# Kernel tuning notes

Measured on AMD Instinct MI355X. Metric: run time of the kernel, lower is better.

Reference implementation:

```python
import jax, jax.numpy as jnp
import numpy as np
import math

B, S, E, H = 2, 2048, 1024, 16
HD = E // H          # head_dim = 64
HX = 64              # helix_dim
P = HX // 2          # helix pairs = 32

def setup_inputs() -> dict:
    key = jax.random.key(0)
    ks = jax.random.split(key, 12)
    sc = 0.02
    return {
        "x":    jax.random.normal(ks[0], (B, S, E), dtype=jnp.float32),
        "Wq":   jax.random.normal(ks[1], (E, E), dtype=jnp.float32) * sc,
        "bq":   jnp.zeros((E,), dtype=jnp.float32),
        "Wk":   jax.random.normal(ks[2], (E, E), dtype=jnp.float32) * sc,
        "bk":   jnp.zeros((E,), dtype=jnp.float32),
        "Wv":   jax.random.normal(ks[3], (E, E), dtype=jnp.float32) * sc,
        "bv":   jnp.zeros((E,), dtype=jnp.float32),
        "Wo":   jax.random.normal(ks[4], (E, E), dtype=jnp.float32) * sc,
        "bo":   jnp.zeros((E,), dtype=jnp.float32),
        "Whel": jax.random.normal(ks[5], (H, HX, HD), dtype=jnp.float32) * sc,
        "bhel": jnp.zeros((H, HX), dtype=jnp.float32),
    }

def _l2norm(x, eps=1e-12):
    # torch F.normalize(p=2, dim=-1): x / max(||x||, eps)
    n = jnp.sqrt(jnp.sum(x * x, axis=-1, keepdims=True))
    return x / jnp.maximum(n, eps)

def _scramble(t):
    # faithful to torch: (B,S,2) -> transpose(1,2) -> reshape(B,S,2),
    # vectorized over (H,P): t is (B,H,P,S,2)
    b, h, p, s, _ = t.shape
    return jnp.swapaxes(t, -1, -2).reshape(b, h, p, s, 2)

def reference(x, Wq, bq, Wk, bk, Wv, bv, Wo, bo, Whel, bhel):
    b, s, e = x.shape
    h, hx, hd = Whel.shape
    p = hx // 2
    q = x @ Wq.T + bq
    k = x @ Wk.T + bk
    v = x @ Wv.T + bv
    qh = q.reshape(b, s, h, hd)
    kh = k.reshape(b, s, h, hd)
    # per-head helical projections: (B,S,H,HX)
    q_hel = jnp.einsum('bshd,hed->bshe', qh, Whel) + bhel
    k_hel = jnp.einsum('bshd,hed->bshe', kh, Whel) + bhel
    # split into 2D coords, normalize each pair: (B,H,P,S,2)
    qn = _l2norm(q_hel.reshape(b, s, h, p, 2)).transpose(0, 2, 3, 1, 4)
    kn = _l2norm(k_hel.reshape(b, s, h, p, 2)).transpose(0, 2, 3, 1, 4)
    qn = _scramble(qn)
    kn = _scramble(kn)
    # helical similarity averaged over pairs: (B,H,S,S)
    helical = jnp.einsum('bhpsc,bhptc->bhst', qn, kn) / p
    # standard scaled dot-product scores
    dot = jnp.einsum('bshd,bthd->bhst', qh, kh) / math.sqrt(hd)
    alpha = 0.5
    attn = jax.nn.softmax(alpha * dot + (1.0 - alpha) * helical, axis=-1)
    vh = v.reshape(b, s, h, hd)
    out = jnp.einsum('bhst,bthd->bshd', attn, vh).reshape(b, s, e)
    return out @ Wo.T + bo
```

## Files before the change

### kernel.cpp

```cpp
#include <hip/hip_runtime.h>
#include <hip/hip_bf16.h>


typedef unsigned short u16;
typedef unsigned int u32;
typedef __attribute__((ext_vector_type(8))) __bf16 bf16x8;
typedef __attribute__((ext_vector_type(4))) float f32x4;
typedef __attribute__((ext_vector_type(16))) float f32x16;

union BFrag { u32 u[4]; bf16x8 b; };

__device__ __forceinline__ u16 f2b(float f) {
  u32 u = __float_as_uint(f);
  u32 r = (u + 0x7fffu + ((u >> 16) & 1u)) >> 16;
  return (u16)r;
}
__device__ __forceinline__ float b2f(u16 h) {
  return __uint_as_float(((u32)h) << 16);
}

__device__ __forceinline__ f32x4 mfma16(bf16x8 a, bf16x8 b, f32x4 c) {
  return __builtin_amdgcn_mfma_f32_16x16x32_bf16(a, b, c, 0, 0, 0);
}
__device__ __forceinline__ f32x16 mfma32(bf16x8 a, bf16x8 b, f32x16 c) {
  return __builtin_amdgcn_mfma_f32_32x32x16_bf16(a, b, c, 0, 0, 0);
}

__device__ __forceinline__ void gld16(void* lds, const void* g) {
  __builtin_amdgcn_global_load_lds(
      (const __attribute__((address_space(1))) unsigned int*)g,
      (__attribute__((address_space(3))) unsigned int*)lds, 16, 0, 0);
}

__device__ __forceinline__ void pl32swap(u32& a, u32& b, int l5) {
#if __has_builtin(__builtin_amdgcn_permlane32_swap)
  typedef unsigned int u32x2v __attribute__((ext_vector_type(2)));
  u32x2v r = __builtin_amdgcn_permlane32_swap(a, b, false, false);
  a = r[0];
  b = r[1];
#else
  u32 ea = __shfl_xor((int)a, 32);
  u32 eb = __shfl_xor((int)b, 32);
  u32 na = l5 ? eb : a;
  u32 nb = l5 ? b : ea;
  a = na;
  b = nb;
#endif
}

#define LOG2E 1.4426950408889634f

#define PIPE_BARRIER(N)                                         \
  do {                                                          \
    __builtin_amdgcn_sched_barrier(0);                          \
    asm volatile("s_waitcnt vmcnt(" #N ")" ::: "memory");       \
    __builtin_amdgcn_s_barrier();                               \
    __builtin_amdgcn_sched_barrier(0);                          \
  } while (0)

__global__ __launch_bounds__(256) void cast_kernel(
    const float* __restrict__ x,  const float* __restrict__ wq,
    const float* __restrict__ wk, const float* __restrict__ wv,
    const float* __restrict__ wo, const float* __restrict__ whel,
    u16* __restrict__ xb, u16* __restrict__ wb, u16* __restrict__ wob,
    u16* __restrict__ whb) {
  long long q = (long long)blockIdx.x * 256 + threadIdx.x;
  const float* s; u16* d; long long base;
  if (q < 1048576)      { s = x;    d = xb;            base = 0; }
  else if (q < 1310720) { s = wq;   d = wb;            base = 1048576; }
  else if (q < 1572864) { s = wk;   d = wb + 1048576;  base = 1310720; }
  else if (q < 1835008) { s = wv;   d = wb + 2097152;  base = 1572864; }
  else if (q < 2097152) { s = wo;   d = wob;           base = 1835008; }
  else                  { s = whel; d = whb;           base = 2097152; }
  long long e = (q - base) * 4;
  float4 v = *(const float4*)(s + e);
  ushort4 o;
  o.x = f2b(v.x); o.y = f2b(v.y); o.z = f2b(v.z); o.w = f2b(v.w);
  *(ushort4*)(d + e) = o;
}

__global__ __launch_bounds__(512, 6) void qkv_gemm(
    const u16* __restrict__ xb, const u16* __restrict__ wb,
    const float* __restrict__ bq, const float* __restrict__ bk,
    const float* __restrict__ bv, const u16* __restrict__ whb,
    const float* __restrict__ bhel,
    u16* __restrict__ Qcat, u16* __restrict__ Kcat, u16* __restrict__ vt) {
  union SM {
    struct { u16 Al[3][128][32]; u16 Bl[3][128][32]; } m;
    struct { u16 T[64][136]; } t;
    struct { u16 Th[4][32][72]; u16 Hs[2][128][64]; } e;
  };
  __shared__ SM sm;
  const int nt = blockIdx.x, mt = blockIdx.y;
  const int which = nt >> 3;
  const int n0 = (nt & 7) << 7;
  const int m0 = mt << 7;
  const int tid = threadIdx.x;
  const int w = tid >> 6, lane = tid & 63;
  const int g = lane >> 4, c15 = lane & 15;
  const int wm = w & 1, hl = (w >> 1) & 1, ch = w >> 2;
  const int nbase = hl * 64 + ch * 32;
  const u16* Wp = wb + (long long)which * (1024 * 1024) + n0 * 1024;
  const u16* Ap = xb + m0 * 1024;
  const int srow = tid >> 2;
  const int scol = (tid & 3) << 3;

  f32x4 acc[4][2];
#pragma unroll
  for (int i = 0; i < 4; i++)
#pragma unroll
    for (int j = 0; j < 2; j++) acc[i][j] = f32x4{0.f, 0.f, 0.f, 0.f};

  gld16(&sm.m.Al[0][srow][scol], Ap + srow * 1024 + scol);
  gld16(&sm.m.Bl[0][srow][scol], Wp + srow * 1024 + scol);
  gld16(&sm.m.Al[1][srow][scol], Ap + srow * 1024 + 32 + scol);
  gld16(&sm.m.Bl[1][srow][scol], Wp + srow * 1024 + 32 + scol);

  int cur = 0;
  for (int it = 0; it < 32; ++it) {
    if (it < 31) { PIPE_BARRIER(2); } else { PIPE_BARRIER(0); }
    if (it + 2 < 32) {
      const int pf = (cur >= 1) ? cur - 1 : 2;
      const int kn = (it + 2) << 5;
      gld16(&sm.m.Al[pf][srow][scol], Ap + srow * 1024 + kn + scol);
      gld16(&sm.m.Bl[pf][srow][scol], Wp + srow * 1024 + kn + scol);
    }
    bf16x8 a[4], b[2];
#pragma unroll
    for (int i = 0; i < 4; i++)
      a[i] = *(const bf16x8*)&sm.m.Al[cur][wm * 64 + i * 16 + c15][g * 8];
#pragma unroll
    for (int j = 0; j < 2; j++)
      b[j] = *(const bf16x8*)&sm.m.Bl[cur][nbase + j * 16 + c15][g * 8];
#pragma unroll
    for (int i = 0; i < 4; i++)
#pragma unroll
      for (int j = 0; j < 2; j++) acc[i][j] = mfma16(a[i], b[j], acc[i][j]);
    cur = (cur == 2) ? 0 : cur + 1;
  }

  if (which == 2) {
#pragma unroll
    for (int half = 0; half < 2; ++half) {
      __syncthreads();
      if (hl == half) {
#pragma unroll
        for (int i = 0; i < 4; i++)
#pragma unroll
          for (int j = 0; j < 2; j++)
#pragma unroll
            for (int r = 0; r < 4; r++) {
              int nloc = ch * 32 + j * 16 + c15;
              int mloc = wm * 64 + i * 16 + g * 4 + r;
              float v = acc[i][j][r] + bv[n0 + half * 64 + nloc];
              sm.t.T[nloc][mloc] = f2b(v);
            }
      }
      __syncthreads();
#pragma unroll
      for (int it = 0; it < 2; ++it) {
        int idx = it * 512 + tid;
        int row = idx >> 4;
        int cm = (idx & 15) * 8;
        int col = n0 + half * 64 + row;
        int hh = col >> 6, dd = col & 63;
        int m = m0 + cm;
        int bb2 = m >> 11, s = m & 2047;
        *(uint4*)&vt[(((bb2 * 16 + hh) * 64) + dd) * 2048 + s] =
            *(const uint4*)&sm.t.T[row][cm];
      }
    }
    return;
  }

  const float* bias = (which == 0) ? bq : bk;
  const float fold = (which == 0) ? (0.0625f * LOG2E) : 1.0f;
  const float osc  = (which == 0) ? (0.125f * LOG2E) : 0.125f;
  const int h0 = n0 >> 6;
  const int hsel = h0 + hl;
  const int pid = hl * 2 + wm;
  u16* Dst = ((which == 0) ? Qcat : Kcat);

  __syncthreads();
  const int bb2 = m0 >> 11;
  const int ubase = (m0 & 2047) >> 1;

#pragma unroll
  for (int half = 0; half < 2; ++half) {
#pragma unroll
    for (int i2 = 0; i2 < 2; ++i2) {
      int i = half * 2 + i2;
#pragma unroll
      for (int j = 0; j < 2; ++j)
#pragma unroll
        for (int r = 0; r < 4; ++r) {
          int row = m0 + wm * 64 + i * 16 + g * 4 + r;
          int d = ch * 32 + j * 16 + c15;
          int col = n0 + hl * 64 + d;
          float vraw = acc[i][j][r] + bias[col];
          int bb = row >> 11, s = row & 2047;
          Dst[(((long long)(bb * 16 + hsel) * 2048) + s) * 128 + d] =
              f2b(vraw * fold);
          sm.e.Th[pid][i2 * 16 + g * 4 + r][d] = f2b(vraw);
        }
    }
    __syncthreads();

    bf16x8 wf[2][4];
#pragma unroll
    for (int kh = 0; kh < 2; ++kh)
#pragma unroll
      for (int nf = 0; nf < 4; ++nf)
        wf[kh][nf] = *(const bf16x8*)(whb + hsel * 4096 +
                                      (nf * 16 + c15) * 64 + kh * 32 + g * 8);

    f32x4 hacc[4];
#pragma unroll
    for (int nf = 0; nf < 4; ++nf) hacc[nf] = f32x4{0.f, 0.f, 0.f, 0.f};
#pragma unroll
    for (int kh = 0; kh < 2; ++kh) {
      bf16x8 a0 = *(const bf16x8*)&sm.e.Th[pid][ch * 16 + c15][kh * 32 + g * 8];
#pragma unroll
      for (int nf = 0; nf < 4; ++nf)
        hacc[nf] = mfma16(a0, wf[kh][nf], hacc[nf]);
    }
#pragma unroll
    for (int nf = 0; nf < 4; ++nf)
#pragma unroll
      for (int r = 0; r < 4; ++r) {
        int e = nf * 16 + c15;
        float v = hacc[nf][r] + bhel[hsel * 64 + e];
        float pp = __shfl_xor(v, 1);
        float nn = sqrtf(v * v + pp * pp);
        float o = v / fmaxf(nn, 1e-12f) * osc;
        int tl = wm * 64 + half * 32 + ch * 16 + g * 4 + r;
        sm.e.Hs[hl][(e & 1) * 64 + (tl >> 1)][(e & ~1) | (tl & 1)] = f2b(o);
      }
    __syncthreads();
  }
#pragma unroll
  for (int it = 0; it < 4; ++it) {
    int idx = it * 512 + tid;
    int hh = idx >> 10;
    int hr = (idx >> 3) & 127;
    int ck = idx & 7;
    int coord = hr >> 6, ul = hr & 63;
    int row_out = coord * 1024 + ubase + ul;
    *(uint4*)&Dst[(((long long)(bb2 * 16 + h0 + hh) * 2048) + row_out) * 128 +
                  64 + ck * 8] = *(const uint4*)&sm.e.Hs[hh][hr][ck * 8];
  }
}

__global__ __launch_bounds__(512, 4) void attn_kernel(
    const u16* __restrict__ Qcat, const u16* __restrict__ Kcat,
    const u16* __restrict__ vt, u16* __restrict__ AO) {
  __shared__ u16 Kl[3][64][128];
  __shared__ u16 Vl[3][64][64];
  __shared__ float denl[2][128];
  const int bh = blockIdx.x, qt = blockIdx.y;
  const int bb = bh >> 4, h = bh & 15;
  const int q0 = qt << 7;
  const int tid = threadIdx.x;
  const int w = tid >> 6, lane = tid & 63;
  const int wq = w & 3, wt = w >> 2;
  const int l31 = lane & 31, l5 = lane >> 5;
  const u16* Qb = Qcat + (long long)bh * (2048 * 128);
  const u16* Kb = Kcat + (long long)bh * (2048 * 128);
  const u16* Vb = vt + (long long)bh * (64 * 2048);

  bf16x8 qf[8];
  {
    const u16* qrow = Qb + (q0 + 32 * wq + l31) * 128 + l5 * 8;
#pragma unroll
    for (int ks = 0; ks < 8; ++ks) qf[ks] = *(const bf16x8*)(qrow + ks * 16);
  }

  const int ll = tid;
  const int krow0 = ll >> 4;
  const int kp = ll & 15;
  const int ksrc0 = (kp & 8) | ((kp & 7) ^ (krow0 & 7));
  const int krow1 = 32 + krow0;
  const int ksrc1 = (kp & 8) | ((kp & 7) ^ (krow1 & 7));
  const int vd = ll >> 3;
  const int vsrc = (ll & 7) ^ (vd & 7);

  gld16(((u16*)Kl[0]) + ll * 8,        Kb + krow0 * 128 + ksrc0 * 8);
  gld16(((u16*)Kl[0]) + 4096 + ll * 8, Kb + krow1 * 128 + ksrc1 * 8);
  gld16(((u16*)Vl[0]) + ll * 8,        Vb + vd * 2048 + vsrc * 8);
  gld16(((u16*)Kl[1]) + ll * 8,        Kb + (64 + krow0) * 128 + ksrc0 * 8);
  gld16(((u16*)Kl[1]) + 4096 + ll * 8, Kb + (64 + krow1) * 128 + ksrc1 * 8);
  gld16(((u16*)Vl[1]) + ll * 8,        Vb + vd * 2048 + 64 + vsrc * 8);

  f32x16 accO0, accO1;
#pragma unroll
  for (int i = 0; i < 16; ++i) { accO0[i] = 0.f; accO1[i] = 0.f; }
  float den = 0.f;

  const int krow = 32 * wt + l31;
  const int kr7 = krow & 7;

  int cur = 0;
  for (int t = 0; t < 32; ++t) {
    if (t < 31) { PIPE_BARRIER(3); } else { PIPE_BARRIER(0); }
    if (t + 2 < 32) {
      const int pf = (cur >= 1) ? cur - 1 : 2;
      const int t2 = (t + 2) << 6;
      u16* Kd = (u16*)Kl[pf];
      gld16(Kd + ll * 8,        Kb + (t2 + krow0) * 128 + ksrc0 * 8);
      gld16(Kd + 4096 + ll * 8, Kb + (t2 + krow1) * 128 + ksrc1 * 8);
      gld16(((u16*)Vl[pf]) + ll * 8, Vb + vd * 2048 + t2 + vsrc * 8);
    }

    f32x16 accS;
#pragma unroll
    for (int i = 0; i < 16; ++i) accS[i] = 0.f;
#pragma unroll
    for (int ks = 0; ks < 8; ++ks) {
      int lc = 2 * ks + l5;
      int p = (lc & 8) | ((lc & 7) ^ kr7);
      bf16x8 ak = *(const bf16x8*)&Kl[cur][krow][p * 8];
      accS = mfma32(ak, qf[ks], accS);
    }

    u32 D0[2], D1[2], D2[2], D3[2];
#pragma unroll
    for (int rr = 0; rr < 4; ++rr) {
      float p0 = __builtin_amdgcn_exp2f(accS[4 * rr + 0]);
      float p1 = __builtin_amdgcn_exp2f(accS[4 * rr + 1]);
      float p2 = __builtin_amdgcn_exp2f(accS[4 * rr + 2]);
      float p3 = __builtin_amdgcn_exp2f(accS[4 * rr + 3]);
      den += (p0 + p1) + (p2 + p3);
      u32 lo = __builtin_amdgcn_perm(__float_as_uint(p1), __float_as_uint(p0),
                                     0x07060302u);
      u32 hi = __builtin_amdgcn_perm(__float_as_uint(p3), __float_as_uint(p2),
                                     0x07060302u);
      if (rr == 0) { D0[0] = lo; D0[1] = hi; }
      else if (rr == 1) { D1[0] = lo; D1[1] = hi; }
      else if (rr == 2) { D2[0] = lo; D2[1] = hi; }
      else { D3[0] = lo; D3[1] = hi; }
    }
    BFrag A0, A1;
    A0.u[0] = D0[0]; A0.u[2] = D1[0]; pl32swap(A0.u[0], A0.u[2], l5);
    A0.u[1] = D0[1]; A0.u[3] = D1[1]; pl32swap(A0.u[1], A0.u[3], l5);
    A1.u[0] = D2[0]; A1.u[2] = D3[0]; pl32swap(A1.u[0], A1.u[2], l5);
    A1.u[1] = D2[1]; A1.u[3] = D3[1]; pl32swap(A1.u[1], A1.u[3], l5);

#pragma unroll
    for (int dq = 0; dq < 2; ++dq) {
      int d = 32 * dq + l31;
      int d7 = d & 7;
#pragma unroll
      for (int ks = 0; ks < 2; ++ks) {
        int lc = 4 * wt + 2 * ks + l5;
        bf16x8 bvf = *(const bf16x8*)&Vl[cur][d][((lc ^ d7) & 7) * 8];
        if (dq == 0) accO0 = mfma32(ks ? A1.b : A0.b, bvf, accO0);
        else         accO1 = mfma32(ks ? A1.b : A0.b, bvf, accO1);
      }
    }
    cur = (cur == 2) ? 0 : cur + 1;
  }

  den += __shfl_xor(den, 32);
  if (lane < 32) denl[wt][32 * wq + lane] = den;
  __syncthreads();

  float* S = (float*)Kl;
  if (wt == 1) {
#pragma unroll
    for (int r = 0; r < 16; ++r) {
      int qr = (r & 3) + 8 * (r >> 2) + 4 * l5;
      S[(wq * 32 + qr) * 64 + l31] = accO0[r];
      S[(wq * 32 + qr) * 64 + 32 + l31] = accO1[r];
    }
  }
  __syncthreads();
  if (wt == 0) {
#pragma unroll
    for (int r = 0; r < 16; ++r) {
      int qr = (r & 3) + 8 * (r >> 2) + 4 * l5;
      int ql = 32 * wq + qr;
      float inv = 1.0f / (denl[0][ql] + denl[1][ql]);
      float o0 = (accO0[r] + S[(wq * 32 + qr) * 64 + l31]) * inv;
      float o1 = (accO1[r] + S[(wq * 32 + qr) * 64 + 32 + l31]) * inv;
      long long base = ((long long)(bb * 2048 + q0 + ql) * 1024) + h * 64;
      AO[base + l31] = f2b(o0);
      AO[base + 32 + l31] = f2b(o1);
    }
  }
}

__global__ __launch_bounds__(256, 4) void out_gemm(
    const u16* __restrict__ AO, const u16* __restrict__ wob,
    const float* __restrict__ bo, float* __restrict__ out) {
  __shared__ u16 Al[3][64][32];
  __shared__ u16 Bl[3][64][32];
  const int n0 = blockIdx.x << 6;
  const int m0 = blockIdx.y << 6;
  const int tid = threadIdx.x;
  const int wave = tid >> 6, lane = tid & 63;
  const int g = lane >> 4, c15 = lane & 15;
  const int wm = wave & 1, wn = wave >> 1;
  const u16* Wp = wob + n0 * 1024;
  const u16* Ap = AO + m0 * 1024;
  const int srow = tid >> 2;
  const int scol = (tid & 3) << 3;

  f32x4 acc[2][2];
#pragma unroll
  for (int i = 0; i < 2; i++)
#pragma unroll
    for (int j = 0; j < 2; j++) acc[i][j] = f32x4{0.f, 0.f, 0.f, 0.f};

  gld16(&Al[0][srow][scol], Ap + srow * 1024 + scol);
  gld16(&Bl[0][srow][scol], Wp + srow * 1024 + scol);
  gld16(&Al[1][srow][scol], Ap + srow * 1024 + 32 + scol);
  gld16(&Bl[1][srow][scol], Wp + srow * 1024 + 32 + scol);

  int cur = 0;
  for (int it = 0; it < 32; ++it) {
    if (it < 31) { PIPE_BARRIER(2); } else { PIPE_BARRIER(0); }
    if (it + 2 < 32) {
      const int pf = (cur >= 1) ? cur - 1 : 2;
      const int kn = (it + 2) << 5;
      gld16(&Al[pf][srow][scol], Ap + srow * 1024 + kn + scol);
      gld16(&Bl[pf][srow][scol], Wp + srow * 1024 + kn + scol);
    }
    bf16x8 a[2], b[2];
#pragma unroll
    for (int i = 0; i < 2; i++)
      a[i] = *(const bf16x8*)&Al[cur][wm * 32 + i * 16 + c15][g * 8];
#pragma unroll
    for (int j = 0; j < 2; j++)
      b[j] = *(const bf16x8*)&Bl[cur][wn * 32 + j * 16 + c15][g * 8];
#pragma unroll
    for (int i = 0; i < 2; i++)
#pragma unroll
      for (int j = 0; j < 2; j++) acc[i][j] = mfma16(a[i], b[j], acc[i][j]);
    cur = (cur == 2) ? 0 : cur + 1;
  }
#pragma unroll
  for (int i = 0; i < 2; i++)
#pragma unroll
    for (int j = 0; j < 2; j++)
#pragma unroll
      for (int r = 0; r < 4; r++) {
        int row = m0 + wm * 32 + i * 16 + g * 4 + r;
        int col = n0 + wn * 32 + j * 16 + c15;
        out[row * 1024 + col] = acc[i][j][r] + bo[col];
      }
}

extern "C" void kernel_launch(void* const* d_in, const int* in_sizes, int n_in,
                              void* d_out, int out_size, void* d_ws,
                              size_t ws_size, hipStream_t stream) {
  const float* x    = (const float*)d_in[0];
  const float* Wq   = (const float*)d_in[1];
  const float* bq   = (const float*)d_in[2];
  const float* Wk   = (const float*)d_in[3];
  const float* bk   = (const float*)d_in[4];
  const float* Wv   = (const float*)d_in[5];
  const float* bv   = (const float*)d_in[6];
  const float* Wo   = (const float*)d_in[7];
  const float* bo   = (const float*)d_in[8];
  const float* Whel = (const float*)d_in[9];
  const float* bhel = (const float*)d_in[10];
  float* out = (float*)d_out;

  char* ws = (char*)d_ws;
  u16* xb   = (u16*)(ws + 0);
  u16* wb   = (u16*)(ws + 8388608);
  u16* wob  = (u16*)(ws + 14680064);
  u16* whb  = (u16*)(ws + 16777216);
  u16* Qcat = (u16*)(ws + 16908288);
  u16* Kcat = (u16*)(ws + 33685504);
  u16* vt   = (u16*)(ws + 50462720);
  u16* AO   = (u16*)(ws + 58851328);

  cast_kernel<<<dim3(8256), dim3(256), 0, stream>>>(x, Wq, Wk, Wv, Wo, Whel,
                                                    xb, wb, wob, whb);
  qkv_gemm<<<dim3(24, 32), dim3(512), 0, stream>>>(xb, wb, bq, bk, bv, whb,
                                                   bhel, Qcat, Kcat, vt);
  attn_kernel<<<dim3(32, 16), dim3(512), 0, stream>>>(Qcat, Kcat, vt, AO);
  out_gemm<<<dim3(16, 64), dim3(256), 0, stream>>>(AO, wob, bo, out);
}
```

Baseline: 220.6 us.

## Process two query sub-tiles per wave in attention to reuse K/V fragments

Halves the attention block to 256 threads, with each wave handling 64 query rows as two 32-row sub-tiles. This lets each K and V LDS fragment feed two MFMAs instead of one. The K/V staging drops from a triple buffer to a double buffer with a full barrier each iteration. The aim is to cut LDS read traffic per FLOP, but it doubles accumulator registers, lowers wave count per block, and exposes more load latency through the shallower pipeline.

```diff
diff --git a/kernel.cpp b/kernel.cpp
--- a/kernel.cpp
+++ b/kernel.cpp
@@ -251,99 +251,137 @@
   }
 }
 
-__global__ __launch_bounds__(512, 4) void attn_kernel(
+__global__ __launch_bounds__(256, 2) void attn_kernel(
     const u16* __restrict__ Qcat, const u16* __restrict__ Kcat,
     const u16* __restrict__ vt, u16* __restrict__ AO) {
-  __shared__ u16 Kl[3][64][128];
-  __shared__ u16 Vl[3][64][64];
+  __shared__ u16 Kl[2][64][128];
+  __shared__ u16 Vl[2][64][64];
   __shared__ float denl[2][128];
   const int bh = blockIdx.x, qt = blockIdx.y;
   const int bb = bh >> 4, h = bh & 15;
   const int q0 = qt << 7;
   const int tid = threadIdx.x;
   const int w = tid >> 6, lane = tid & 63;
-  const int wq = w & 3, wt = w >> 2;
+  const int wq = w & 1, wt = w >> 1;
   const int l31 = lane & 31, l5 = lane >> 5;
   const u16* Qb = Qcat + (long long)bh * (2048 * 128);
   const u16* Kb = Kcat + (long long)bh * (2048 * 128);
   const u16* Vb = vt + (long long)bh * (64 * 2048);
 
-  bf16x8 qf[8];
+  bf16x8 qf0[8], qf1[8];
   {
-    const u16* qrow = Qb + (q0 + 32 * wq + l31) * 128 + l5 * 8;
-#pragma unroll
-    for (int ks = 0; ks < 8; ++ks) qf[ks] = *(const bf16x8*)(qrow + ks * 16);
-  }
-
-  const int ll = tid;
-  const int krow0 = ll >> 4;
-  const int kp = ll & 15;
-  const int ksrc0 = (kp & 8) | ((kp & 7) ^ (krow0 & 7));
-  const int krow1 = 32 + krow0;
-  const int ksrc1 = (kp & 8) | ((kp & 7) ^ (krow1 & 7));
-  const int vd = ll >> 3;
-  const int vsrc = (ll & 7) ^ (vd & 7);
-
-  gld16(((u16*)Kl[0]) + ll * 8,        Kb + krow0 * 128 + ksrc0 * 8);
-  gld16(((u16*)Kl[0]) + 4096 + ll * 8, Kb + krow1 * 128 + ksrc1 * 8);
-  gld16(((u16*)Vl[0]) + ll * 8,        Vb + vd * 2048 + vsrc * 8);
-  gld16(((u16*)Kl[1]) + ll * 8,        Kb + (64 + krow0) * 128 + ksrc0 * 8);
-  gld16(((u16*)Kl[1]) + 4096 + ll * 8, Kb + (64 + krow1) * 128 + ksrc1 * 8);
-  gld16(((u16*)Vl[1]) + ll * 8,        Vb + vd * 2048 + 64 + vsrc * 8);
-
-  f32x16 accO0, accO1;
-#pragma unroll
-  for (int i = 0; i < 16; ++i) { accO0[i] = 0.f; accO1[i] = 0.f; }
-  float den = 0.f;
+    const u16* qrow0 = Qb + (q0 + 64 * wq + l31) * 128 + l5 * 8;
+    const u16* qrow1 = qrow0 + 32 * 128;
+#pragma unroll
+    for (int ks = 0; ks < 8; ++ks) {
+      qf0[ks] = *(const bf16x8*)(qrow0 + ks * 16);
+      qf1[ks] = *(const bf16x8*)(qrow1 + ks * 16);
+    }
+  }
+
+  const int kp = tid & 15;
+  int krowp[4], ksrcp[4];
+#pragma unroll
+  for (int p = 0; p < 4; ++p) {
+    krowp[p] = p * 16 + (tid >> 4);
+    ksrcp[p] = (kp & 8) | ((kp & 7) ^ (krowp[p] & 7));
+  }
+  const int vc = tid & 7;
+  int vdp[2], vsrcp[2];
+#pragma unroll
+  for (int p = 0; p < 2; ++p) {
+    vdp[p] = p * 32 + (tid >> 3);
+    vsrcp[p] = vc ^ (vdp[p] & 7);
+  }
+
+#define STAGE_TILE(buf, t1)                                                  \
+  do {                                                                       \
+    u16* Kd = (u16*)Kl[buf];                                                 \
+    u16* Vd = (u16*)Vl[buf];                                                 \
+    _Pragma("unroll") for (int p = 0; p < 4; ++p)                            \
+        gld16(Kd + (p * 256 + tid) * 8,                                      \
+              Kb + ((t1) + krowp[p]) * 128 + ksrcp[p] * 8);                  \
+    _Pragma("unroll") for (int p = 0; p < 2; ++p)                            \
+        gld16(Vd + (p * 256 + tid) * 8,                                      \
+              Vb + vdp[p] * 2048 + (t1) + vsrcp[p] * 8);                     \
+  } while (0)
+
+  STAGE_TILE(0, 0);
+
+  f32x16 accO00, accO01, accO10, accO11;
+#pragma unroll
+  for (int i = 0; i < 16; ++i) {
+    accO00[i] = 0.f; accO01[i] = 0.f; accO10[i] = 0.f; accO11[i] = 0.f;
+  }
+  float den0 = 0.f, den1 = 0.f;
 
   const int krow = 32 * wt + l31;
   const int kr7 = krow & 7;
 
-  int cur = 0;
   for (int t = 0; t < 32; ++t) {
-    if (t < 31) { PIPE_BARRIER(3); } else { PIPE_BARRIER(0); }
-    if (t + 2 < 32) {
-      const int pf = (cur >= 1) ? cur - 1 : 2;
-      const int t2 = (t + 2) << 6;
-      u16* Kd = (u16*)Kl[pf];
-      gld16(Kd + ll * 8,        Kb + (t2 + krow0) * 128 + ksrc0 * 8);
-      gld16(Kd + 4096 + ll * 8, Kb + (t2 + krow1) * 128 + ksrc1 * 8);
-      gld16(((u16*)Vl[pf]) + ll * 8, Vb + vd * 2048 + t2 + vsrc * 8);
-    }
-
-    f32x16 accS;
-#pragma unroll
-    for (int i = 0; i < 16; ++i) accS[i] = 0.f;
+    const int cur = t & 1;
+    PIPE_BARRIER(0);
+    if (t + 1 < 32) { STAGE_TILE(cur ^ 1, (t + 1) << 6); }
+
+    f32x16 accS0, accS1;
+#pragma unroll
+    for (int i = 0; i < 16; ++i) { accS0[i] = 0.f; accS1[i] = 0.f; }
 #pragma unroll
     for (int ks = 0; ks < 8; ++ks) {
       int lc = 2 * ks + l5;
       int p = (lc & 8) | ((lc & 7) ^ kr7);
       bf16x8 ak = *(const bf16x8*)&Kl[cur][krow][p * 8];
-      accS = mfma32(ak, qf[ks], accS);
-    }
-
-    u32 D0[2], D1[2], D2[2], D3[2];
-#pragma unroll
-    for (int rr = 0; rr < 4; ++rr) {
-      float p0 = __builtin_amdgcn_exp2f(accS[4 * rr + 0]);
-      float p1 = __builtin_amdgcn_exp2f(accS[4 * rr + 1]);
-      float p2 = __builtin_amdgcn_exp2f(accS[4 * rr + 2]);
-      float p3 = __builtin_amdgcn_exp2f(accS[4 * rr + 3]);
-      den += (p0 + p1) + (p2 + p3);
-      u32 lo = __builtin_amdgcn_perm(__float_as_uint(p1), __float_as_uint(p0),
-                                     0x07060302u);
-      u32 hi = __builtin_amdgcn_perm(__float_as_uint(p3), __float_as_uint(p2),
-                                     0x07060302u);
-      if (rr == 0) { D0[0] = lo; D0[1] = hi; }
-      else if (rr == 1) { D1[0] = lo; D1[1] = hi; }
-      else if (rr == 2) { D2[0] = lo; D2[1] = hi; }
-      else { D3[0] = lo; D3[1] = hi; }
-    }
-    BFrag A0, A1;
-    A0.u[0] = D0[0]; A0.u[2] = D1[0]; pl32swap(A0.u[0], A0.u[2], l5);
-    A0.u[1] = D0[1]; A0.u[3] = D1[1]; pl32swap(A0.u[1], A0.u[3], l5);
-    A1.u[0] = D2[0]; A1.u[2] = D3[0]; pl32swap(A1.u[0], A1.u[2], l5);
-    A1.u[1] = D2[1]; A1.u[3] = D3[1]; pl32swap(A1.u[1], A1.u[3], l5);
+      accS0 = mfma32(ak, qf0[ks], accS0);
+      accS1 = mfma32(ak, qf1[ks], accS1);
+    }
+
+    BFrag A0q0, A1q0, A0q1, A1q1;
+    {
+      u32 D0[2], D1[2], D2[2], D3[2];
+#pragma unroll
+      for (int rr = 0; rr < 4; ++rr) {
+        float p0 = __builtin_amdgcn_exp2f(accS0[4 * rr + 0]);
+        float p1 = __builtin_amdgcn_exp2f(accS0[4 * rr + 1]);
+        float p2 = __builtin_amdgcn_exp2f(accS0[4 * rr + 2]);
+        float p3 = __builtin_amdgcn_exp2f(accS0[4 * rr + 3]);
+        den0 += (p0 + p1) + (p2 + p3);
+        u32 lo = __builtin_amdgcn_perm(__float_as_uint(p1),
+                                       __float_as_uint(p0), 0x07060302u);
+        u32 hi = __builtin_amdgcn_perm(__float_as_uint(p3),
+                                       __float_as_uint(p2), 0x07060302u);
+        if (rr == 0) { D0[0] = lo; D0[1] = hi; }
+        else if (rr == 1) { D1[0] = lo; D1[1] = hi; }
+        else if (rr == 2) { D2[0] = lo; D2[1] = hi; }
+        else { D3[0] = lo; D3[1] = hi; }
+      }
+      A0q0.u[0] = D0[0]; A0q0.u[2] = D1[0]; pl32swap(A0q0.u[0], A0q0.u[2], l5);
+      A0q0.u[1] = D0[1]; A0q0.u[3] = D1[1]; pl32swap(A0q0.u[1], A0q0.u[3], l5);
+      A1q0.u[0] = D2[0]; A1q0.u[2] = D3[0]; pl32swap(A1q0.u[0], A1q0.u[2], l5);
+      A1q0.u[1] = D2[1]; A1q0.u[3] = D3[1]; pl32swap(A1q0.u[1], A1q0.u[3], l5);
+    }
+    {
+      u32 D0[2], D1[2], D2[2], D3[2];
+#pragma unroll
+      for (int rr = 0; rr < 4; ++rr) {
+        float p0 = __builtin_amdgcn_exp2f(accS1[4 * rr + 0]);
+        float p1 = __builtin_amdgcn_exp2f(accS1[4 * rr + 1]);
+        float p2 = __builtin_amdgcn_exp2f(accS1[4 * rr + 2]);
+        float p3 = __builtin_amdgcn_exp2f(accS1[4 * rr + 3]);
+        den1 += (p0 + p1) + (p2 + p3);
+        u32 lo = __builtin_amdgcn_perm(__float_as_uint(p1),
+                                       __float_as_uint(p0), 0x07060302u);
+        u32 hi = __builtin_amdgcn_perm(__float_as_uint(p3),
+                                       __float_as_uint(p2), 0x07060302u);
+        if (rr == 0) { D0[0] = lo; D0[1] = hi; }
+        else if (rr == 1) { D1[0] = lo; D1[1] = hi; }
+        else if (rr == 2) { D2[0] = lo; D2[1] = hi; }
+        else { D3[0] = lo; D3[1] = hi; }
+      }
+      A0q1.u[0] = D0[0]; A0q1.u[2] = D1[0]; pl32swap(A0q1.u[0], A0q1.u[2], l5);
+      A0q1.u[1] = D0[1]; A0q1.u[3] = D1[1]; pl32swap(A0q1.u[1], A0q1.u[3], l5);
+      A1q1.u[0] = D2[0]; A1q1.u[2] = D3[0]; pl32swap(A1q1.u[0], A1q1.u[2], l5);
+      A1q1.u[1] = D2[1]; A1q1.u[3] = D3[1]; pl32swap(A1q1.u[1], A1q1.u[3], l5);
+    }
 
 #pragma unroll
     for (int dq = 0; dq < 2; ++dq) {
@@ -353,39 +391,55 @@
       for (int ks = 0; ks < 2; ++ks) {
         int lc = 4 * wt + 2 * ks + l5;
         bf16x8 bvf = *(const bf16x8*)&Vl[cur][d][((lc ^ d7) & 7) * 8];
-        if (dq == 0) accO0 = mfma32(ks ? A1.b : A0.b, bvf, accO0);
-        else         accO1 = mfma32(ks ? A1.b : A0.b, bvf, accO1);
-      }
-    }
-    cur = (cur == 2) ? 0 : cur + 1;
-  }
-
-  den += __shfl_xor(den, 32);
-  if (lane < 32) denl[wt][32 * wq + lane] = den;
+        if (dq == 0) {
+          accO00 = mfma32(ks ? A1q0.b : A0q0.b, bvf, accO00);
+          accO10 = mfma32(ks ? A1q1.b : A0q1.b, bvf, accO10);
+        } else {
+          accO01 = mfma32(ks ? A1q0.b : A0q0.b, bvf, accO01);
+          accO11 = mfma32(ks ? A1q1.b : A0q1.b, bvf, accO11);
+        }
+      }
+    }
+  }
+#undef STAGE_TILE
+
+  den0 += __shfl_xor(den0, 32);
+  den1 += __shfl_xor(den1, 32);
+  if (lane < 32) {
+    denl[wt][64 * wq + lane] = den0;
+    denl[wt][64 * wq + 32 + lane] = den1;
+  }
   __syncthreads();
 
-  float* S = (float*)Kl;
+  float* Ssc = (float*)Kl;
   if (wt == 1) {
 #pragma unroll
-    for (int r = 0; r < 16; ++r) {
-      int qr = (r & 3) + 8 * (r >> 2) + 4 * l5;
-      S[(wq * 32 + qr) * 64 + l31] = accO0[r];
-      S[(wq * 32 + qr) * 64 + 32 + l31] = accO1[r];
-    }
+    for (int qs = 0; qs < 2; ++qs)
+#pragma unroll
+      for (int r = 0; r < 16; ++r) {
+        int qr = (r & 3) + 8 * (r >> 2) + 4 * l5;
+        int ql = 64 * wq + 32 * qs + qr;
+        Ssc[ql * 64 + l31]      = qs ? accO10[r] : accO00[r];
+        Ssc[ql * 64 + 32 + l31] = qs ? accO11[r] : accO01[r];
+      }
   }
   __syncthreads();
   if (wt == 0) {
 #pragma unroll
-    for (int r = 0; r < 16; ++r) {
-      int qr = (r & 3) + 8 * (r >> 2) + 4 * l5;
-      int ql = 32 * wq + qr;
-      float inv = 1.0f / (denl[0][ql] + denl[1][ql]);
-      float o0 = (accO0[r] + S[(wq * 32 + qr) * 64 + l31]) * inv;
-      float o1 = (accO1[r] + S[(wq * 32 + qr) * 64 + 32 + l31]) * inv;
-      long long base = ((long long)(bb * 2048 + q0 + ql) * 1024) + h * 64;
-      AO[base + l31] = f2b(o0);
-      AO[base + 32 + l31] = f2b(o1);
-    }
+    for (int qs = 0; qs < 2; ++qs)
+#pragma unroll
+      for (int r = 0; r < 16; ++r) {
+        int qr = (r & 3) + 8 * (r >> 2) + 4 * l5;
+        int ql = 64 * wq + 32 * qs + qr;
+        float inv = 1.0f / (denl[0][ql] + denl[1][ql]);
+        float m0v = qs ? accO10[r] : accO00[r];
+        float m1v = qs ? accO11[r] : accO01[r];
+        float o0 = (m0v + Ssc[ql * 64 + l31]) * inv;
+        float o1 = (m1v + Ssc[ql * 64 + 32 + l31]) * inv;
+        long long base = ((long long)(bb * 2048 + q0 + ql) * 1024) + h * 64;
+        AO[base + l31] = f2b(o0);
+        AO[base + 32 + l31] = f2b(o1);
+      }
   }
 }
 
@@ -480,6 +534,6 @@
                                                     xb, wb, wob, whb);
   qkv_gemm<<<dim3(24, 32), dim3(512), 0, stream>>>(xb, wb, bq, bk, bv, whb,
                                                    bhel, Qcat, Kcat, vt);
-  attn_kernel<<<dim3(32, 16), dim3(512), 0, stream>>>(Qcat, Kcat, vt, AO);
+  attn_kernel<<<dim3(32, 16), dim3(256), 0, stream>>>(Qcat, Kcat, vt, AO);
   out_gemm<<<dim3(16, 64), dim3(256), 0, stream>>>(AO, wob, bo, out);
 }
```

Measured after the change: 222.9 us. Within noise of the previous version (+1.0%).
